# Performance work log

Measured on AMD Instinct MI355X. Metric: run time of the kernel, lower is better.

## Reference

```python
import jax, jax.numpy as jnp
import numpy as np
from jax import lax

B, T, D = 8, 2048, 1024


def setup_inputs() -> dict:
    key = jax.random.key(0)
    ks = jax.random.split(key, 8)
    s = 1.0 / np.sqrt(D)
    x = jax.random.normal(ks[0], (B, T, D), dtype=jnp.float32)
    Wq = jax.random.uniform(ks[1], (D, D), jnp.float32, -s, s)
    bq = jax.random.uniform(ks[2], (D,), jnp.float32, -s, s)
    Wk = jax.random.uniform(ks[3], (D, D), jnp.float32, -s, s)
    bk = jax.random.uniform(ks[4], (D,), jnp.float32, -s, s)
    Wv = jax.random.uniform(ks[5], (D, D), jnp.float32, -s, s)
    bv = jax.random.uniform(ks[6], (D,), jnp.float32, -s, s)
    decay = jnp.full((D,), 0.9, dtype=jnp.float32)  # nn.Parameter(ones*0.9)
    return {"x": x, "Wq": Wq, "bq": bq, "Wk": Wk, "bk": bk,
            "Wv": Wv, "bv": bv, "decay": decay}


def reference(x, Wq, bq, Wk, bk, Wv, bv, decay):
    # projections (torch Linear: x @ W.T + b)
    q = jnp.einsum('btd,ed->bte', x, Wq) + bq
    k = jnp.einsum('btd,ed->bte', x, Wk) + bk
    v = jnp.einsum('btd,ed->bte', x, Wv) + bv
    kv = k * v  # [B,T,D]

    # diagonal-decay linear recurrence: mem_t = decay * mem_{t-1} + kv_t
    def step(mem, kv_t):
        mem = decay * mem + kv_t  # [B,D]
        return mem, mem

    mem0 = jnp.zeros((B, D), dtype=x.dtype)
    _, mems = lax.scan(step, mem0, jnp.swapaxes(kv, 0, 1))  # mems: [T,B,D]
    out = q * jnp.swapaxes(mems, 0, 1)  # output_t = q_t * mem_t
    return out
```

## Files before the change

### kernel.cpp

```cpp
#include <hip/hip_runtime.h>
#include <cstdint>

typedef unsigned short ushort_t;
typedef __bf16 bf16x8 __attribute__((ext_vector_type(8)));
typedef float f32x4 __attribute__((ext_vector_type(4)));

#define B_ 8
#define T_ 2048
#define D_ 1024
#define M_ (B_ * T_)
#define NCHUNK 64
#define CHUNKLEN 32

__device__ __forceinline__ ushort_t f2bf(float f) {
    union { float f; uint32_t u; } v; v.f = f;
    uint32_t u = v.u;
    uint32_t r = (u + 0x7fffu + ((u >> 16) & 1u)) >> 16;
    return (ushort_t)r;
}
__device__ __forceinline__ float bf2f(ushort_t h) {
    union { uint32_t u; float f; } v; v.u = ((uint32_t)h) << 16;
    return v.f;
}

__device__ __forceinline__ void async16(const ushort_t* g, ushort_t* l) {
    __builtin_amdgcn_global_load_lds(
        (const __attribute__((address_space(1))) void*)g,
        (__attribute__((address_space(3))) void*)l, 16, 0, 0);
}

__global__ __launch_bounds__(256) void cast_bf16(const float* __restrict__ src,
                                                 ushort_t* __restrict__ dst, int n4) {
    int i = blockIdx.x * blockDim.x + threadIdx.x;
    if (i < n4) {
        float4 v = ((const float4*)src)[i];
        ushort4 o;
        o.x = f2bf(v.x); o.y = f2bf(v.y); o.z = f2bf(v.z); o.w = f2bf(v.w);
        ((ushort4*)dst)[i] = o;
    }
}

__global__ __launch_bounds__(256) void cast_w3(const float* __restrict__ wq,
                                               const float* __restrict__ wk,
                                               const float* __restrict__ wv,
                                               ushort_t* __restrict__ dst) {
    const int n4 = D_ * D_ / 4;
    int i = blockIdx.x * blockDim.x + threadIdx.x;
    const float* src = (i < n4) ? wq : ((i < 2 * n4) ? wk : wv);
    int li = (i < n4) ? i : ((i < 2 * n4) ? i - n4 : i - 2 * n4);
    float4 v = ((const float4*)src)[li];
    ushort4 o;
    o.x = f2bf(v.x); o.y = f2bf(v.y); o.z = f2bf(v.z); o.w = f2bf(v.w);
    ((ushort4*)(dst))[i] = o;
}

__global__ __launch_bounds__(256) void gemm_q(
    const ushort_t* __restrict__ xb, const ushort_t* __restrict__ Wq,
    const float* __restrict__ bq, ushort_t* __restrict__ qb) {
    __shared__ ushort_t As[128 * 32];
    __shared__ ushort_t Bs[128 * 32];

    const int m0 = blockIdx.x * 128, n0 = blockIdx.y * 128;
    const int t = threadIdx.x;
    const int lane = t & 63, wv = t >> 6;
    const int wr = (wv >> 1) * 64, wc = (wv & 1) * 64;

    f32x4 acc[4][4];
#pragma unroll
    for (int i = 0; i < 4; ++i)
#pragma unroll
        for (int j = 0; j < 4; ++j) acc[i][j] = (f32x4){0.f, 0.f, 0.f, 0.f};

    const int r0 = t >> 2, r1 = r0 + 64;
    const int sc = ((t & 3) ^ ((r0 >> 1) & 3)) * 8;

    const int swq = ((lane & 15) >> 1) & 3;
    const int csel = (((lane >> 4) ^ swq)) * 8;
    const int rowa = wr + (lane & 15);
    const int rowb = wc + (lane & 15);

    for (int kt = 0; kt < 32; ++kt) {
        const int k0 = kt * 32;
        async16(xb + (size_t)(m0 + r0) * D_ + k0 + sc, &As[t * 8]);
        async16(xb + (size_t)(m0 + r1) * D_ + k0 + sc, &As[(t + 256) * 8]);
        async16(Wq + (size_t)(n0 + r0) * D_ + k0 + sc, &Bs[t * 8]);
        async16(Wq + (size_t)(n0 + r1) * D_ + k0 + sc, &Bs[(t + 256) * 8]);
        __syncthreads();

        bf16x8 af[4], bfr[4];
#pragma unroll
        for (int i = 0; i < 4; ++i)
            af[i] = *(const bf16x8*)&As[(rowa + i * 16) * 32 + csel];
#pragma unroll
        for (int j = 0; j < 4; ++j)
            bfr[j] = *(const bf16x8*)&Bs[(rowb + j * 16) * 32 + csel];
#pragma unroll
        for (int i = 0; i < 4; ++i)
#pragma unroll
            for (int j = 0; j < 4; ++j)
                acc[i][j] = __builtin_amdgcn_mfma_f32_16x16x32_bf16(
                    af[i], bfr[j], acc[i][j], 0, 0, 0);
        __syncthreads();
    }

    const int colq = lane & 15;
    const int rowq = (lane >> 4) * 4;
#pragma unroll
    for (int i = 0; i < 4; ++i) {
#pragma unroll
        for (int j = 0; j < 4; ++j) {
            const int cg = n0 + wc + j * 16 + colq;
            const float bval = bq[cg];
#pragma unroll
            for (int r = 0; r < 4; ++r) {
                const int rg = m0 + wr + i * 16 + rowq + r;
                qb[(size_t)rg * D_ + cg] = f2bf(acc[i][j][r] + bval);
            }
        }
    }
}

__global__ __launch_bounds__(256, 2) void gemm_kv(
    const ushort_t* __restrict__ xb, const ushort_t* __restrict__ Wk,
    const ushort_t* __restrict__ Wv, const float* __restrict__ bk,
    const float* __restrict__ bv, ushort_t* __restrict__ kvb) {
    __shared__ ushort_t As[128 * 32];
    __shared__ ushort_t Bk[128 * 32];
    __shared__ ushort_t Bv[128 * 32];

    const int m0 = blockIdx.x * 128, n0 = blockIdx.y * 128;
    const int t = threadIdx.x;
    const int lane = t & 63, wv = t >> 6;
    const int wr = (wv >> 1) * 64, wc = (wv & 1) * 64;

    f32x4 acck[4][4], accv[4][4];
#pragma unroll
    for (int i = 0; i < 4; ++i)
#pragma unroll
        for (int j = 0; j < 4; ++j) {
            acck[i][j] = (f32x4){0.f, 0.f, 0.f, 0.f};
            accv[i][j] = (f32x4){0.f, 0.f, 0.f, 0.f};
        }

    const int r0 = t >> 2, r1 = r0 + 64;
    const int sc = ((t & 3) ^ ((r0 >> 1) & 3)) * 8;

    const int swq = ((lane & 15) >> 1) & 3;
    const int csel = (((lane >> 4) ^ swq)) * 8;
    const int rowa = wr + (lane & 15);
    const int rowb = wc + (lane & 15);

    for (int kt = 0; kt < 32; ++kt) {
        const int k0 = kt * 32;
        async16(xb + (size_t)(m0 + r0) * D_ + k0 + sc, &As[t * 8]);
        async16(xb + (size_t)(m0 + r1) * D_ + k0 + sc, &As[(t + 256) * 8]);
        async16(Wk + (size_t)(n0 + r0) * D_ + k0 + sc, &Bk[t * 8]);
        async16(Wk + (size_t)(n0 + r1) * D_ + k0 + sc, &Bk[(t + 256) * 8]);
        async16(Wv + (size_t)(n0 + r0) * D_ + k0 + sc, &Bv[t * 8]);
        async16(Wv + (size_t)(n0 + r1) * D_ + k0 + sc, &Bv[(t + 256) * 8]);
        __syncthreads();

        bf16x8 af[4], bk8[4], bv8[4];
#pragma unroll
        for (int i = 0; i < 4; ++i)
            af[i] = *(const bf16x8*)&As[(rowa + i * 16) * 32 + csel];
#pragma unroll
        for (int j = 0; j < 4; ++j) {
            bk8[j] = *(const bf16x8*)&Bk[(rowb + j * 16) * 32 + csel];
            bv8[j] = *(const bf16x8*)&Bv[(rowb + j * 16) * 32 + csel];
        }
#pragma unroll
        for (int i = 0; i < 4; ++i)
#pragma unroll
            for (int j = 0; j < 4; ++j) {
                acck[i][j] = __builtin_amdgcn_mfma_f32_16x16x32_bf16(
                    af[i], bk8[j], acck[i][j], 0, 0, 0);
                accv[i][j] = __builtin_amdgcn_mfma_f32_16x16x32_bf16(
                    af[i], bv8[j], accv[i][j], 0, 0, 0);
            }
        __syncthreads();
    }

    const int colq = lane & 15;
    const int rowq = (lane >> 4) * 4;
#pragma unroll
    for (int i = 0; i < 4; ++i) {
#pragma unroll
        for (int j = 0; j < 4; ++j) {
            const int cg = n0 + wc + j * 16 + colq;
            const float bkv = bk[cg], bvv = bv[cg];
#pragma unroll
            for (int r = 0; r < 4; ++r) {
                const int rg = m0 + wr + i * 16 + rowq + r;
                const float kf = acck[i][j][r] + bkv;
                const float vf = accv[i][j][r] + bvv;
                kvb[(size_t)rg * D_ + cg] = f2bf(kf * vf);
            }
        }
    }
}

__global__ __launch_bounds__(256) void scan_chunks(
    const ushort_t* __restrict__ kvb, const float* __restrict__ decay,
    float* __restrict__ S) {
    const int b = blockIdx.x >> 7;
    const int c = (blockIdx.x >> 1) & 63;
    const int dg = blockIdx.x & 1;
    const int d0 = dg * 512 + threadIdx.x * 2;
    const float dc0 = decay[d0], dc1 = decay[d0 + 1];
    float m0 = 0.f, m1 = 0.f;
    size_t base = ((size_t)b * T_ + c * CHUNKLEN) * D_ + d0;
#pragma unroll 8
    for (int i = 0; i < CHUNKLEN; ++i) {
        ushort2 kv = *(const ushort2*)&kvb[base + (size_t)i * D_];
        m0 = fmaf(dc0, m0, bf2f(kv.x));
        m1 = fmaf(dc1, m1, bf2f(kv.y));
    }
    float2* so = (float2*)&S[((size_t)b * NCHUNK + c) * D_ + d0];
    *so = make_float2(m0, m1);
}

__global__ __launch_bounds__(256) void scan_carry(
    const float* __restrict__ S, const float* __restrict__ decay,
    float* __restrict__ P) {
    const int idx = blockIdx.x * blockDim.x + threadIdx.x;
    const int d = idx & (D_ - 1), b = idx >> 10;
    const float dec = decay[d];
    float dL = dec;
    dL *= dL; dL *= dL; dL *= dL; dL *= dL; dL *= dL;
    float p = 0.f;
    for (int c = 0; c < NCHUNK; ++c) {
        const size_t o = ((size_t)b * NCHUNK + c) * D_ + d;
        P[o] = p;
        p = fmaf(dL, p, S[o]);
    }
}

__global__ __launch_bounds__(256) void scan_final(
    const ushort_t* __restrict__ kvb, const ushort_t* __restrict__ qb,
    const float* __restrict__ decay, const float* __restrict__ P,
    float* __restrict__ out) {
    const int b = blockIdx.x >> 7;
    const int c = (blockIdx.x >> 1) & 63;
    const int dg = blockIdx.x & 1;
    const int d0 = dg * 512 + threadIdx.x * 2;
    const float dc0 = decay[d0], dc1 = decay[d0 + 1];
    const float2 p2 = *(const float2*)&P[((size_t)b * NCHUNK + c) * D_ + d0];
    float m0 = p2.x, m1 = p2.y;
    size_t base = ((size_t)b * T_ + c * CHUNKLEN) * D_ + d0;
#pragma unroll 8
    for (int i = 0; i < CHUNKLEN; ++i) {
        const size_t o = base + (size_t)i * D_;
        ushort2 kv = *(const ushort2*)&kvb[o];
        ushort2 q2 = *(const ushort2*)&qb[o];
        m0 = fmaf(dc0, m0, bf2f(kv.x));
        m1 = fmaf(dc1, m1, bf2f(kv.y));
        *(float2*)&out[o] = make_float2(bf2f(q2.x) * m0, bf2f(q2.y) * m1);
    }
}

extern "C" void kernel_launch(void* const* d_in, const int* in_sizes, int n_in,
                              void* d_out, int out_size, void* d_ws, size_t ws_size,
                              hipStream_t stream) {
    const float* x     = (const float*)d_in[0];
    const float* Wq    = (const float*)d_in[1];
    const float* bq    = (const float*)d_in[2];
    const float* Wk    = (const float*)d_in[3];
    const float* bk    = (const float*)d_in[4];
    const float* Wv    = (const float*)d_in[5];
    const float* bv    = (const float*)d_in[6];
    const float* decay = (const float*)d_in[7];
    float* out = (float*)d_out;

    char* ws = (char*)d_ws;
    ushort_t* xb  = (ushort_t*)(ws);
    ushort_t* Wb  = (ushort_t*)(ws + 33554432);
    ushort_t* qb  = (ushort_t*)(ws + 39845888);
    ushort_t* kvb = (ushort_t*)(ws + 73400320);
    float*    S   = (float*)(ws);
    float*    P   = (float*)(ws + 2097152);

    ushort_t* Wkb = Wb + D_ * D_;
    ushort_t* Wvb = Wb + 2 * D_ * D_;

    cast_bf16<<<(M_ * D_ / 4 + 255) / 256, 256, 0, stream>>>(x, xb, M_ * D_ / 4);
    cast_w3<<<(3 * D_ * D_ / 4) / 256, 256, 0, stream>>>(Wq, Wk, Wv, Wb);

    dim3 g(M_ / 128, 8);
    gemm_q<<<g, 256, 0, stream>>>(xb, Wb, bq, qb);
    gemm_kv<<<g, 256, 0, stream>>>(xb, Wkb, Wvb, bk, bv, kvb);

    scan_chunks<<<B_ * NCHUNK * 2, 256, 0, stream>>>(kvb, decay, S);
    scan_carry<<<(B_ * D_) / 256, 256, 0, stream>>>(S, decay, P);
    scan_final<<<B_ * NCHUNK * 2, 256, 0, stream>>>(kvb, qb, decay, P, out);
}
```

Baseline: 289.6 us.

## Merge cast kernels, widen Q GEMM tile to 128x256, vectorize scan kernels

The x and weight casts are merged into one launch. The Q projection GEMM now computes two 128-column output tiles per block, sharing the A tile and doubling MFMA work per LDS load of A. The scan kernels switch from 2 to 4 channels per thread, using float4 and ushort4 loads and stores, and launch half as many blocks. The larger Q tile raises register use (two accumulator sets) and halves the grid, which may hurt occupancy.

```diff
diff --git a/kernel.cpp b/kernel.cpp
--- a/kernel.cpp
+++ b/kernel.cpp
@@ -29,47 +29,48 @@
         (__attribute__((address_space(3))) void*)l, 16, 0, 0);
 }
 
-__global__ __launch_bounds__(256) void cast_bf16(const float* __restrict__ src,
-                                                 ushort_t* __restrict__ dst, int n4) {
+__global__ __launch_bounds__(256) void cast_all(
+    const float* __restrict__ x, const float* __restrict__ wq,
+    const float* __restrict__ wk, const float* __restrict__ wv,
+    ushort_t* __restrict__ xb, ushort_t* __restrict__ Wb) {
+    const int nx4 = M_ * D_ / 4, nw4 = D_ * D_ / 4;
     int i = blockIdx.x * blockDim.x + threadIdx.x;
-    if (i < n4) {
-        float4 v = ((const float4*)src)[i];
-        ushort4 o;
-        o.x = f2bf(v.x); o.y = f2bf(v.y); o.z = f2bf(v.z); o.w = f2bf(v.w);
-        ((ushort4*)dst)[i] = o;
-    }
-}
-
-__global__ __launch_bounds__(256) void cast_w3(const float* __restrict__ wq,
-                                               const float* __restrict__ wk,
-                                               const float* __restrict__ wv,
-                                               ushort_t* __restrict__ dst) {
-    const int n4 = D_ * D_ / 4;
-    int i = blockIdx.x * blockDim.x + threadIdx.x;
-    const float* src = (i < n4) ? wq : ((i < 2 * n4) ? wk : wv);
-    int li = (i < n4) ? i : ((i < 2 * n4) ? i - n4 : i - 2 * n4);
-    float4 v = ((const float4*)src)[li];
+    const float* src; ushort_t* dstp; int si;
+    if (i < nx4) {
+        src = x; si = i; dstp = xb + (size_t)i * 4;
+    } else {
+        int j = i - nx4;
+        dstp = Wb + (size_t)j * 4;
+        if (j < nw4)          { src = wq; si = j; }
+        else if (j < 2 * nw4) { src = wk; si = j - nw4; }
+        else                  { src = wv; si = j - 2 * nw4; }
+    }
+    float4 v = ((const float4*)src)[si];
     ushort4 o;
     o.x = f2bf(v.x); o.y = f2bf(v.y); o.z = f2bf(v.z); o.w = f2bf(v.w);
-    ((ushort4*)(dst))[i] = o;
-}
-
-__global__ __launch_bounds__(256) void gemm_q(
+    *(ushort4*)dstp = o;
+}
+
+__global__ __launch_bounds__(256, 2) void gemm_q2(
     const ushort_t* __restrict__ xb, const ushort_t* __restrict__ Wq,
     const float* __restrict__ bq, ushort_t* __restrict__ qb) {
     __shared__ ushort_t As[128 * 32];
-    __shared__ ushort_t Bs[128 * 32];
-
-    const int m0 = blockIdx.x * 128, n0 = blockIdx.y * 128;
+    __shared__ ushort_t B0[128 * 32];
+    __shared__ ushort_t B1[128 * 32];
+
+    const int m0 = blockIdx.x * 128, n0 = blockIdx.y * 256;
     const int t = threadIdx.x;
     const int lane = t & 63, wv = t >> 6;
     const int wr = (wv >> 1) * 64, wc = (wv & 1) * 64;
 
-    f32x4 acc[4][4];
+    f32x4 acc0[4][4], acc1[4][4];
 #pragma unroll
     for (int i = 0; i < 4; ++i)
 #pragma unroll
-        for (int j = 0; j < 4; ++j) acc[i][j] = (f32x4){0.f, 0.f, 0.f, 0.f};
+        for (int j = 0; j < 4; ++j) {
+            acc0[i][j] = (f32x4){0.f, 0.f, 0.f, 0.f};
+            acc1[i][j] = (f32x4){0.f, 0.f, 0.f, 0.f};
+        }
 
     const int r0 = t >> 2, r1 = r0 + 64;
     const int sc = ((t & 3) ^ ((r0 >> 1) & 3)) * 8;
@@ -83,23 +84,30 @@
         const int k0 = kt * 32;
         async16(xb + (size_t)(m0 + r0) * D_ + k0 + sc, &As[t * 8]);
         async16(xb + (size_t)(m0 + r1) * D_ + k0 + sc, &As[(t + 256) * 8]);
-        async16(Wq + (size_t)(n0 + r0) * D_ + k0 + sc, &Bs[t * 8]);
-        async16(Wq + (size_t)(n0 + r1) * D_ + k0 + sc, &Bs[(t + 256) * 8]);
+        async16(Wq + (size_t)(n0 + r0) * D_ + k0 + sc, &B0[t * 8]);
+        async16(Wq + (size_t)(n0 + r1) * D_ + k0 + sc, &B0[(t + 256) * 8]);
+        async16(Wq + (size_t)(n0 + 128 + r0) * D_ + k0 + sc, &B1[t * 8]);
+        async16(Wq + (size_t)(n0 + 128 + r1) * D_ + k0 + sc, &B1[(t + 256) * 8]);
         __syncthreads();
 
-        bf16x8 af[4], bfr[4];
+        bf16x8 af[4], b08[4], b18[4];
 #pragma unroll
         for (int i = 0; i < 4; ++i)
             af[i] = *(const bf16x8*)&As[(rowa + i * 16) * 32 + csel];
 #pragma unroll
-        for (int j = 0; j < 4; ++j)
-            bfr[j] = *(const bf16x8*)&Bs[(rowb + j * 16) * 32 + csel];
+        for (int j = 0; j < 4; ++j) {
+            b08[j] = *(const bf16x8*)&B0[(rowb + j * 16) * 32 + csel];
+            b18[j] = *(const bf16x8*)&B1[(rowb + j * 16) * 32 + csel];
+        }
 #pragma unroll
         for (int i = 0; i < 4; ++i)
 #pragma unroll
-            for (int j = 0; j < 4; ++j)
-                acc[i][j] = __builtin_amdgcn_mfma_f32_16x16x32_bf16(
-                    af[i], bfr[j], acc[i][j], 0, 0, 0);
+            for (int j = 0; j < 4; ++j) {
+                acc0[i][j] = __builtin_amdgcn_mfma_f32_16x16x32_bf16(
+                    af[i], b08[j], acc0[i][j], 0, 0, 0);
+                acc1[i][j] = __builtin_amdgcn_mfma_f32_16x16x32_bf16(
+                    af[i], b18[j], acc1[i][j], 0, 0, 0);
+            }
         __syncthreads();
     }
 
@@ -109,12 +117,14 @@
     for (int i = 0; i < 4; ++i) {
 #pragma unroll
         for (int j = 0; j < 4; ++j) {
-            const int cg = n0 + wc + j * 16 + colq;
-            const float bval = bq[cg];
+            const int cg0 = n0 + wc + j * 16 + colq;
+            const int cg1 = cg0 + 128;
+            const float bv0 = bq[cg0], bv1 = bq[cg1];
 #pragma unroll
             for (int r = 0; r < 4; ++r) {
                 const int rg = m0 + wr + i * 16 + rowq + r;
-                qb[(size_t)rg * D_ + cg] = f2bf(acc[i][j][r] + bval);
+                qb[(size_t)rg * D_ + cg0] = f2bf(acc0[i][j][r] + bv0);
+                qb[(size_t)rg * D_ + cg1] = f2bf(acc1[i][j][r] + bv1);
             }
         }
     }
@@ -203,21 +213,21 @@
 __global__ __launch_bounds__(256) void scan_chunks(
     const ushort_t* __restrict__ kvb, const float* __restrict__ decay,
     float* __restrict__ S) {
-    const int b = blockIdx.x >> 7;
-    const int c = (blockIdx.x >> 1) & 63;
-    const int dg = blockIdx.x & 1;
-    const int d0 = dg * 512 + threadIdx.x * 2;
-    const float dc0 = decay[d0], dc1 = decay[d0 + 1];
-    float m0 = 0.f, m1 = 0.f;
+    const int b = blockIdx.x >> 6;
+    const int c = blockIdx.x & 63;
+    const int d0 = threadIdx.x * 4;
+    const float4 dc = *(const float4*)&decay[d0];
+    float m0 = 0.f, m1 = 0.f, m2 = 0.f, m3 = 0.f;
     size_t base = ((size_t)b * T_ + c * CHUNKLEN) * D_ + d0;
 #pragma unroll 8
     for (int i = 0; i < CHUNKLEN; ++i) {
-        ushort2 kv = *(const ushort2*)&kvb[base + (size_t)i * D_];
-        m0 = fmaf(dc0, m0, bf2f(kv.x));
-        m1 = fmaf(dc1, m1, bf2f(kv.y));
-    }
-    float2* so = (float2*)&S[((size_t)b * NCHUNK + c) * D_ + d0];
-    *so = make_float2(m0, m1);
+        ushort4 kv = *(const ushort4*)&kvb[base + (size_t)i * D_];
+        m0 = fmaf(dc.x, m0, bf2f(kv.x));
+        m1 = fmaf(dc.y, m1, bf2f(kv.y));
+        m2 = fmaf(dc.z, m2, bf2f(kv.z));
+        m3 = fmaf(dc.w, m3, bf2f(kv.w));
+    }
+    *(float4*)&S[((size_t)b * NCHUNK + c) * D_ + d0] = make_float4(m0, m1, m2, m3);
 }
 
 __global__ __launch_bounds__(256) void scan_carry(
@@ -240,22 +250,24 @@
     const ushort_t* __restrict__ kvb, const ushort_t* __restrict__ qb,
     const float* __restrict__ decay, const float* __restrict__ P,
     float* __restrict__ out) {
-    const int b = blockIdx.x >> 7;
-    const int c = (blockIdx.x >> 1) & 63;
-    const int dg = blockIdx.x & 1;
-    const int d0 = dg * 512 + threadIdx.x * 2;
-    const float dc0 = decay[d0], dc1 = decay[d0 + 1];
-    const float2 p2 = *(const float2*)&P[((size_t)b * NCHUNK + c) * D_ + d0];
-    float m0 = p2.x, m1 = p2.y;
+    const int b = blockIdx.x >> 6;
+    const int c = blockIdx.x & 63;
+    const int d0 = threadIdx.x * 4;
+    const float4 dc = *(const float4*)&decay[d0];
+    const float4 p4 = *(const float4*)&P[((size_t)b * NCHUNK + c) * D_ + d0];
+    float m0 = p4.x, m1 = p4.y, m2 = p4.z, m3 = p4.w;
     size_t base = ((size_t)b * T_ + c * CHUNKLEN) * D_ + d0;
 #pragma unroll 8
     for (int i = 0; i < CHUNKLEN; ++i) {
         const size_t o = base + (size_t)i * D_;
-        ushort2 kv = *(const ushort2*)&kvb[o];
-        ushort2 q2 = *(const ushort2*)&qb[o];
-        m0 = fmaf(dc0, m0, bf2f(kv.x));
-        m1 = fmaf(dc1, m1, bf2f(kv.y));
-        *(float2*)&out[o] = make_float2(bf2f(q2.x) * m0, bf2f(q2.y) * m1);
+        ushort4 kv = *(const ushort4*)&kvb[o];
+        ushort4 q4 = *(const ushort4*)&qb[o];
+        m0 = fmaf(dc.x, m0, bf2f(kv.x));
+        m1 = fmaf(dc.y, m1, bf2f(kv.y));
+        m2 = fmaf(dc.z, m2, bf2f(kv.z));
+        m3 = fmaf(dc.w, m3, bf2f(kv.w));
+        *(float4*)&out[o] = make_float4(bf2f(q4.x) * m0, bf2f(q4.y) * m1,
+                                        bf2f(q4.z) * m2, bf2f(q4.w) * m3);
     }
 }
 
@@ -280,17 +292,17 @@
     float*    S   = (float*)(ws);
     float*    P   = (float*)(ws + 2097152);
 
+    ushort_t* Wqb = Wb;
     ushort_t* Wkb = Wb + D_ * D_;
     ushort_t* Wvb = Wb + 2 * D_ * D_;
 
-    cast_bf16<<<(M_ * D_ / 4 + 255) / 256, 256, 0, stream>>>(x, xb, M_ * D_ / 4);
-    cast_w3<<<(3 * D_ * D_ / 4) / 256, 256, 0, stream>>>(Wq, Wk, Wv, Wb);
-
-    dim3 g(M_ / 128, 8);
-    gemm_q<<<g, 256, 0, stream>>>(xb, Wb, bq, qb);
-    gemm_kv<<<g, 256, 0, stream>>>(xb, Wkb, Wvb, bk, bv, kvb);
-
-    scan_chunks<<<B_ * NCHUNK * 2, 256, 0, stream>>>(kvb, decay, S);
+    const int ncast = (M_ * D_ / 4) + (3 * D_ * D_ / 4);
+    cast_all<<<ncast / 256, 256, 0, stream>>>(x, Wq, Wk, Wv, xb, Wb);
+
+    gemm_q2<<<dim3(M_ / 128, D_ / 256), 256, 0, stream>>>(xb, Wqb, bq, qb);
+    gemm_kv<<<dim3(M_ / 128, D_ / 128), 256, 0, stream>>>(xb, Wkb, Wvb, bk, bv, kvb);
+
+    scan_chunks<<<B_ * NCHUNK, 256, 0, stream>>>(kvb, decay, S);
     scan_carry<<<(B_ * D_) / 256, 256, 0, stream>>>(S, decay, P);
-    scan_final<<<B_ * NCHUNK * 2, 256, 0, stream>>>(kvb, qb, decay, P, out);
-}
+    scan_final<<<B_ * NCHUNK, 256, 0, stream>>>(kvb, qb, decay, P, out);
+}
```

New measurement: 278.5 us. 3.8% less time.
